# Performance work log

Hardware: AMD Instinct MI355X
Metric: run time of the kernel (lower is better)

Reference implementation:

```python
import jax, jax.numpy as jnp
from jax import lax
import numpy as np

HID = 64      # hidden_size
IND = 25      # input_dim = 10 static + 15 dynamic features
HW = 25       # spatial size fixed by fc1 = Linear(12*12*hidden, ...)


def setup_inputs() -> dict:
    key = jax.random.key(0)
    ks = jax.random.split(key, 8)
    def rn(k, shape, s=0.05):
        return jax.random.normal(k, shape, dtype=jnp.float32) * s
    B, T = 64, 24
    return {
        "x": jax.random.normal(ks[0], (B, T, IND, HW, HW), dtype=jnp.float32),
        "ln_g": jnp.ones((IND,), jnp.float32),
        "ln_b": jnp.zeros((IND,), jnp.float32),
        "w_lstm1": rn(ks[1], (4 * HID, IND + HID, 3, 3)),
        "b_lstm1": jnp.zeros((4 * HID,), jnp.float32),
        "w_lstm2": rn(ks[2], (4 * HID, IND + HID, 3, 3)),
        "b_lstm2": jnp.zeros((4 * HID,), jnp.float32),
        "w_conv": rn(ks[3], (HID, 2 * HID, 3, 3)),
        "b_conv": jnp.zeros((HID,), jnp.float32),
        "w_fc1": rn(ks[4], (HID, 12 * 12 * HID)),
        "b_fc1": jnp.zeros((HID,), jnp.float32),
        "w_fc2": rn(ks[5], (HID // 2, HID)),
        "b_fc2": jnp.zeros((HID // 2,), jnp.float32),
        "w_fc3": rn(ks[6], (2, HID // 2)),
        "b_fc3": jnp.zeros((2,), jnp.float32),
    }


def _convlstm(x, w, b, dil):
    # x: (B, T, C, H, W); one ConvLSTM layer, zero-initialized states.
    # Gate order i, f, o, g (standard ndrplz ConvLSTM); same-padding 3x3 conv
    # with rhs dilation `dil` (padding = dil keeps HxW).
    B, _, _, H, W = x.shape
    h0 = jnp.zeros((B, HID, H, W), x.dtype)

    def step(carry, xt):
        h, c = carry
        z = lax.conv_general_dilated(
            jnp.concatenate([xt, h], axis=1), w, (1, 1),
            [(dil, dil), (dil, dil)], rhs_dilation=(dil, dil))
        z = z + b[None, :, None, None]
        i, f, o, g = jnp.split(z, 4, axis=1)
        c = jax.nn.sigmoid(f) * c + jax.nn.sigmoid(i) * jnp.tanh(g)
        h = jax.nn.sigmoid(o) * jnp.tanh(c)
        return (h, c), None

    (h, _), _ = lax.scan(step, (h0, h0), jnp.moveaxis(x, 1, 0))
    return h  # final hidden state (B, HID, H, W)


def reference(x, ln_g, ln_b, w_lstm1, b_lstm1, w_lstm2, b_lstm2,
              w_conv, b_conv, w_fc1, b_fc1, w_fc2, b_fc2, w_fc3, b_fc3):
    # LayerNorm over the channel dim (torch permutes C to last, LN, permutes back)
    mu = jnp.mean(x, axis=2, keepdims=True)
    var = jnp.var(x, axis=2, keepdims=True)
    xn = (x - mu) * lax.rsqrt(var + 1e-5)
    xn = xn * ln_g[None, None, :, None, None] + ln_b[None, None, :, None, None]

    h1 = _convlstm(xn, w_lstm1, b_lstm1, 1)   # dilation 1 branch
    h2 = _convlstm(xn, w_lstm2, b_lstm2, 2)   # dilation 2 branch
    h = jnp.concatenate([h1, h2], axis=1)     # (B, 2*HID, 25, 25)

    h = lax.conv_general_dilated(h, w_conv, (1, 1), [(1, 1), (1, 1)])
    h = jax.nn.relu(h + b_conv[None, :, None, None])
    # max_pool2d(2): floor(25/2)=12 -> VALID window 2 stride 2
    h = lax.reduce_window(h, -jnp.inf, lax.max, (1, 1, 2, 2), (1, 1, 2, 2), 'VALID')
    h = h.reshape(h.shape[0], -1)             # (B, 12*12*HID), channel-major like torch
    h = jax.nn.relu(h @ w_fc1.T + b_fc1)      # dropout is identity at inference
    h = jax.nn.relu(h @ w_fc2.T + b_fc2)
    h = h @ w_fc3.T + b_fc3
    return jax.nn.log_softmax(h, axis=1)
```

## Files before the change

### kernel.cpp

```cpp
#include <hip/hip_runtime.h>
#include <hip/hip_bf16.h>
#include <math.h>

#define B_    64
#define T_    24
#define IND_  25
#define HID_  64
#define NPIX  625

#define WP0   27
#define WP1   29
#define XSTR  32
#define HSTR  72
#define XROWS0 744
#define XROWS1 856
#define HROWS0 744
#define HROWS1 856
#define XB0   (XROWS0*XSTR)
#define XB1   (XROWS1*XSTR)
#define HB0   (HROWS0*HSTR)
#define HB1   (HROWS1*HSTR)
#define XB0T  (B_*XB0)
#define XB1T  (B_*XB1)
#define HB0T  (B_*HB0)
#define HB1T  (B_*HB1)
#define UEND  (XB0T+XB1T+2*(HB0T+HB1T))

#define RST0  200
#define RST1  272
#define CH0   (RST0*9)
#define CH1   (RST1*9)

#define HCROWS 832
#define HCB    (HCROWS*128)
#define HCTOT  (B_*HCB)

#define WFRAG_PER_BR (9*3*4*4*512)
#define WFRAG_TOT    (2*WFRAG_PER_BR)

typedef __bf16 bf16x8 __attribute__((ext_vector_type(8)));
typedef float  f32x4  __attribute__((ext_vector_type(4)));
typedef unsigned short ushort_t;
typedef unsigned int   uint_t;

typedef const __attribute__((address_space(1))) void as1_cvoid;
typedef __attribute__((address_space(3))) void as3_void;

__device__ __forceinline__ float sigmoidf_(float x) { return 1.f / (1.f + __expf(-x)); }
__device__ __forceinline__ float tanh_fast(float x) { return 2.f / (1.f + __expf(-2.f * x)) - 1.f; }
__device__ __forceinline__ ushort_t f2bf(float f) {
    unsigned int u = __float_as_uint(f);
    u += 0x7FFFu + ((u >> 16) & 1u);
    return (ushort_t)(u >> 16);
}
__device__ __forceinline__ float bf2f(ushort_t h) {
    return __uint_as_float(((unsigned int)h) << 16);
}

__global__ __launch_bounds__(256) void fill_zero_kernel(uint_t* __restrict__ p, int n) {
    int i = blockIdx.x * 256 + threadIdx.x;
    if (i < n) p[i] = 0u;
}

__global__ __launch_bounds__(256) void repack_w_kernel(
    const float* __restrict__ w1, const float* __restrict__ w2, ushort_t* __restrict__ Wfrag)
{
    int id = blockIdx.x * 256 + threadIdx.x;
    if (id >= WFRAG_TOT) return;
    int e    = id & 7;
    int lane = (id >> 3) & 63;
    int mf   = (id >> 9) & 3;
    int wm   = (id >> 11) & 3;
    int rest = id >> 13;
    int kk   = rest % 3;
    int tap  = (rest / 3) % 9;
    int br   = rest / 27;
    int l16 = lane & 15, kh = lane >> 4;
    int gate = mf;
    int oc   = wm * 16 + l16;
    int k    = kh * 8 + e;
    int c;
    if (kk == 0)      c = (k < IND_) ? k : -1;
    else if (kk == 1) c = IND_ + k;
    else              c = IND_ + 32 + k;
    const float* w = br ? w2 : w1;
    float v = (c >= 0) ? w[((size_t)(gate * 64 + oc) * 89 + c) * 9 + tap] : 0.f;
    Wfrag[id] = f2bf(v);
}

__global__ __launch_bounds__(256) void repack_wc_kernel(
    const float* __restrict__ wc, ushort_t* __restrict__ Wc)
{
    int id = blockIdx.x * 256 + threadIdx.x;
    if (id >= 9 * 64 * 128) return;
    int k   = id % 128;
    int oc  = (id / 128) % 64;
    int tap = id / (128 * 64);
    Wc[id] = f2bf(wc[((size_t)(oc * 128) + k) * 9 + tap]);
}

__global__ __launch_bounds__(256) void ln_t_kernel(
    const float* __restrict__ x, const float* __restrict__ gamma, const float* __restrict__ beta,
    ushort_t* __restrict__ xb0, ushort_t* __restrict__ xb1, int t)
{
    int p = blockIdx.x * 256 + threadIdx.x;
    if (p >= B_ * NPIX) return;
    int b = p / NPIX, hw = p % NPIX;
    int y = hw / 25, xx = hw % 25;
    const float* xp = x + ((size_t)(b * T_ + t) * IND_) * NPIX + hw;
    float v[IND_];
    float s = 0.f;
#pragma unroll
    for (int c = 0; c < IND_; ++c) { v[c] = xp[c * NPIX]; s += v[c]; }
    float mu = s * (1.f / IND_);
    float ss = 0.f;
#pragma unroll
    for (int c = 0; c < IND_; ++c) { float d = v[c] - mu; ss += d * d; }
    float rstd = rsqrtf(ss * (1.f / IND_) + 1e-5f);
    ushort_t* o0 = xb0 + (size_t)b * XB0 + (size_t)((y + 1) * WP0 + (xx + 1)) * XSTR;
    ushort_t* o1 = xb1 + (size_t)b * XB1 + (size_t)((y + 2) * WP1 + (xx + 2)) * XSTR;
#pragma unroll
    for (int c = 0; c < IND_; ++c) {
        ushort_t hv = f2bf((v[c] - mu) * rstd * gamma[c] + beta[c]);
        o0[c] = hv;
        o1[c] = hv;
    }
}

__global__ __launch_bounds__(512) void convlstm_mfma_kernel(
    const ushort_t* __restrict__ xb0g, const ushort_t* __restrict__ xb1g,
    const ushort_t* __restrict__ h0c, const ushort_t* __restrict__ h1c,
    ushort_t* __restrict__ h0n, ushort_t* __restrict__ h1n,
    const ushort_t* __restrict__ Wfrag,
    const float* __restrict__ bias1, const float* __restrict__ bias2,
    float* __restrict__ cst, int t)
{
    const int rg = blockIdx.x;
    const int b  = blockIdx.y;
    const int br = blockIdx.z;
    const int d  = 1 + br;
    const int Wp = br ? WP1 : WP0;
    const ushort_t* __restrict__ xb = (br ? xb1g + (size_t)b * XB1 : xb0g + (size_t)b * XB0);
    const ushort_t* __restrict__ hc = (br ? h1c + (size_t)b * HB1 : h0c + (size_t)b * HB0);
    ushort_t* __restrict__ hn       = (br ? h1n + (size_t)b * HB1 : h0n + (size_t)b * HB0);
    const float* __restrict__ bias = br ? bias2 : bias1;
    const ushort_t* __restrict__ WFb = Wfrag + (size_t)br * WFRAG_PER_BR;

    __shared__ ushort_t tile[RST1 * HSTR];

    const int tid = threadIdx.x;
    const int u0  = rg * 5 * Wp;
    const int CH  = br ? CH1 : CH0;

    {
        const char* gsrc = (const char*)(hc + (size_t)u0 * HSTR);
        const int wave_u = tid & 448;
#pragma unroll
        for (int j = 0; j < 5; ++j) {
            const int i = j * 512 + tid;
            if (i < CH) {
                __builtin_amdgcn_global_load_lds(
                    (as1_cvoid*)(gsrc + (size_t)i * 16),
                    (as3_void*)((char*)tile + (size_t)(j * 512 + wave_u) * 16),
                    16, 0, 0);
            }
        }
    }
    __syncthreads();

    const int w    = tid >> 6, lane = tid & 63;
    const int wm   = w & 3, wn = w >> 2;
    const int l16  = lane & 15, kh = lane >> 4;
    const int koff = kh * 8;

    f32x4 acc[4][5];
#pragma unroll
    for (int i = 0; i < 4; ++i)
#pragma unroll
        for (int j = 0; j < 5; ++j) acc[i][j] = (f32x4){0.f, 0.f, 0.f, 0.f};

    int baserel[5];
#pragma unroll
    for (int nf = 0; nf < 5; ++nf) {
        int n = wn * 80 + nf * 16 + l16;
        baserel[nf] = (n >> 5) * Wp + (n & 31);
    }

    for (int tap = 0; tap < 9; ++tap) {
        const int ky = tap / 3, kx = tap - 3 * ky;
        const int toff = (ky * Wp + kx) * d;
        const ushort_t* __restrict__ WT = WFb + (size_t)(tap * 3) * 8192 + wm * 2048 + lane * 8;

        {
            bf16x8 af[4], bfr[5];
#pragma unroll
            for (int mf = 0; mf < 4; ++mf)
                af[mf] = *(const bf16x8*)(WT + mf * 512);
#pragma unroll
            for (int nf = 0; nf < 5; ++nf)
                bfr[nf] = *(const bf16x8*)(xb + (size_t)(u0 + baserel[nf] + toff) * XSTR + koff);
#pragma unroll
            for (int mf = 0; mf < 4; ++mf)
#pragma unroll
                for (int nf = 0; nf < 5; ++nf)
                    acc[mf][nf] = __builtin_amdgcn_mfma_f32_16x16x32_bf16(
                        af[mf], bfr[nf], acc[mf][nf], 0, 0, 0);
        }
#pragma unroll
        for (int kkh = 0; kkh < 2; ++kkh) {
            bf16x8 af[4], bfr[5];
#pragma unroll
            for (int mf = 0; mf < 4; ++mf)
                af[mf] = *(const bf16x8*)(WT + (size_t)(kkh + 1) * 8192 + mf * 512);
#pragma unroll
            for (int nf = 0; nf < 5; ++nf)
                bfr[nf] = *(const bf16x8*)(tile + (baserel[nf] + toff) * HSTR + kkh * 32 + koff);
#pragma unroll
            for (int mf = 0; mf < 4; ++mf)
#pragma unroll
                for (int nf = 0; nf < 5; ++nf)
                    acc[mf][nf] = __builtin_amdgcn_mfma_f32_16x16x32_bf16(
                        af[mf], bfr[nf], acc[mf][nf], 0, 0, 0);
        }
    }

    const int oc0 = wm * 16 + kh * 4;
    float bi4[4], bf4[4], bo4[4], bg4[4];
#pragma unroll
    for (int r = 0; r < 4; ++r) {
        bi4[r] = bias[oc0 + r];
        bf4[r] = bias[64 + oc0 + r];
        bo4[r] = bias[128 + oc0 + r];
        bg4[r] = bias[192 + oc0 + r];
    }
#pragma unroll
    for (int nf = 0; nf < 5; ++nf) {
        const int n = wn * 80 + nf * 16 + l16;
        const int xx = n & 31;
        if (xx >= 25) continue;
        const int y = rg * 5 + (n >> 5);
        const int pix = y * 25 + xx;
        const size_t cbase = ((size_t)((br * B_ + b) * HID_) + oc0) * NPIX + pix;
        ushort_t hs[4];
#pragma unroll
        for (int r = 0; r < 4; ++r) {
            const float zi = acc[0][nf][r] + bi4[r];
            const float zf = acc[1][nf][r] + bf4[r];
            const float zo = acc[2][nf][r] + bo4[r];
            const float zg = acc[3][nf][r] + bg4[r];
            float co = 0.f;
            if (t != 0) co = cst[cbase + (size_t)r * NPIX];
            const float cn = sigmoidf_(zf) * co + sigmoidf_(zi) * tanh_fast(zg);
            cst[cbase + (size_t)r * NPIX] = cn;
            hs[r] = f2bf(sigmoidf_(zo) * tanh_fast(cn));
        }
        uint2 hv;
        hv.x = (uint_t)hs[0] | ((uint_t)hs[1] << 16);
        hv.y = (uint_t)hs[2] | ((uint_t)hs[3] << 16);
        *(uint2*)(hn + (size_t)((y + d) * Wp + (xx + d)) * HSTR + oc0) = hv;
    }
}

__global__ __launch_bounds__(256) void combine_h_kernel(
    const ushort_t* __restrict__ h0, const ushort_t* __restrict__ h1, ushort_t* __restrict__ Hc)
{
    int id = blockIdx.x * 256 + threadIdx.x;
    if (id >= B_ * NPIX * 128) return;
    int k   = id % 128;
    int pix = (id / 128) % NPIX;
    int b   = id / (128 * NPIX);
    int y = pix / 25, xx = pix % 25;
    ushort_t v;
    if (k < 64) v = h0[(size_t)b * HB0 + (size_t)((y + 1) * WP0 + (xx + 1)) * HSTR + k];
    else        v = h1[(size_t)b * HB1 + (size_t)((y + 2) * WP1 + (xx + 2)) * HSTR + (k - 64)];
    Hc[(size_t)b * HCB + (size_t)((y + 1) * 27 + (xx + 1)) * 128 + k] = v;
}

__global__ __launch_bounds__(512) void conv_mfma_kernel(
    const ushort_t* __restrict__ Hc, const ushort_t* __restrict__ Wc,
    const float* __restrict__ bc, float* __restrict__ conv_out)
{
    const int rg = blockIdx.x;
    const int b  = blockIdx.y;
    const ushort_t* __restrict__ Hb = Hc + (size_t)b * HCB;

    const int tid  = threadIdx.x;
    const int w    = tid >> 6, lane = tid & 63;
    const int wm   = w & 1, wn = w >> 1;
    const int l16  = lane & 15, kh = lane >> 4;
    const int koff = kh * 8;

    f32x4 acc[2][2];
#pragma unroll
    for (int i = 0; i < 2; ++i)
#pragma unroll
        for (int j = 0; j < 2; ++j) acc[i][j] = (f32x4){0.f, 0.f, 0.f, 0.f};

    int baserow[2];
#pragma unroll
    for (int nf = 0; nf < 2; ++nf) {
        int n = wn * 32 + nf * 16 + l16;
        baserow[nf] = (rg * 4 + (n >> 5)) * 27 + (n & 31);
    }
    const ushort_t* __restrict__ Wm = Wc + (size_t)(wm * 32 + l16) * 128 + koff;

    for (int tap = 0; tap < 9; ++tap) {
        const int ky = tap / 3, kx = tap - 3 * ky;
        const int toff = ky * 27 + kx;
        const ushort_t* __restrict__ Wt = Wm + (size_t)tap * (64 * 128);
        const ushort_t* Urow[2];
#pragma unroll
        for (int nf = 0; nf < 2; ++nf)
            Urow[nf] = Hb + (size_t)(baserow[nf] + toff) * 128 + koff;
#pragma unroll
        for (int kk = 0; kk < 4; ++kk) {
            bf16x8 af[2], bfr[2];
#pragma unroll
            for (int mf = 0; mf < 2; ++mf)
                af[mf] = *(const bf16x8*)(Wt + mf * 16 * 128 + kk * 32);
#pragma unroll
            for (int nf = 0; nf < 2; ++nf)
                bfr[nf] = *(const bf16x8*)(Urow[nf] + kk * 32);
#pragma unroll
            for (int mf = 0; mf < 2; ++mf)
#pragma unroll
                for (int nf = 0; nf < 2; ++nf)
                    acc[mf][nf] = __builtin_amdgcn_mfma_f32_16x16x32_bf16(
                        af[mf], bfr[nf], acc[mf][nf], 0, 0, 0);
        }
    }

#pragma unroll
    for (int mf = 0; mf < 2; ++mf) {
#pragma unroll
        for (int nf = 0; nf < 2; ++nf) {
            const int n = wn * 32 + nf * 16 + l16;
            const int xx = n & 31;
            if (xx >= 25) continue;
            const int y = rg * 4 + wn;
            if (y >= 25) continue;
#pragma unroll
            for (int r = 0; r < 4; ++r) {
                const int oc = wm * 32 + mf * 16 + kh * 4 + r;
                const float v = fmaxf(acc[mf][nf][r] + bc[oc], 0.f);
                conv_out[((size_t)(b * 64 + oc)) * NPIX + y * 25 + xx] = v;
            }
        }
    }
}

__global__ __launch_bounds__(256) void pool_kernel(
    const float* __restrict__ conv_out, float* __restrict__ pool)
{
    int id = blockIdx.x * 256 + threadIdx.x;
    if (id >= B_ * 64 * 144) return;
    int px = id % 12;
    int py = (id / 12) % 12;
    int oc = (id / 144) % 64;
    int b  = id / (144 * 64);
    const float* p = conv_out + ((size_t)(b * 64 + oc)) * NPIX;
    const int cy = 2 * py, cx = 2 * px;
    float mx = fmaxf(fmaxf(p[cy * 25 + cx], p[cy * 25 + cx + 1]),
                     fmaxf(p[(cy + 1) * 25 + cx], p[(cy + 1) * 25 + cx + 1]));
    pool[(size_t)b * 9216 + oc * 144 + py * 12 + px] = mx;
}

__global__ __launch_bounds__(256) void fc1_kernel(
    const float* __restrict__ pool, const float* __restrict__ w1, const float* __restrict__ b1,
    float* __restrict__ f1)
{
    const int task = blockIdx.x * 4 + (threadIdx.x >> 6);
    const int lane = threadIdx.x & 63;
    const int b = task >> 6, oc = task & 63;
    const float* pr = pool + (size_t)b * 9216;
    const float* wr = w1 + (size_t)oc * 9216;
    float acc = 0.f;
#pragma unroll 4
    for (int it = 0; it < 36; ++it) {
        const int k = it * 256 + lane * 4;
        const float4 p = *(const float4*)(pr + k);
        const float4 ww = *(const float4*)(wr + k);
        acc += p.x * ww.x + p.y * ww.y + p.z * ww.z + p.w * ww.w;
    }
#pragma unroll
    for (int off = 32; off > 0; off >>= 1) acc += __shfl_down(acc, off);
    if (lane == 0) f1[b * 64 + oc] = fmaxf(acc + b1[oc], 0.f);
}

__global__ __launch_bounds__(64) void head2_kernel(
    const float* __restrict__ f1,
    const float* __restrict__ w2, const float* __restrict__ b2,
    const float* __restrict__ w3, const float* __restrict__ b3,
    float* __restrict__ out)
{
    const int b = blockIdx.x;
    __shared__ float f1l[64];
    __shared__ float f2[32];
    const int tid = threadIdx.x;
    f1l[tid] = f1[b * 64 + tid];
    __syncthreads();
    if (tid < 32) {
        float acc = b2[tid];
        const float* wr = w2 + (size_t)tid * 64;
#pragma unroll
        for (int k = 0; k < 64; ++k) acc += f1l[k] * wr[k];
        f2[tid] = fmaxf(acc, 0.f);
    }
    __syncthreads();
    if (tid == 0) {
        float y0 = b3[0], y1 = b3[1];
#pragma unroll
        for (int k = 0; k < 32; ++k) { y0 += f2[k] * w3[k]; y1 += f2[k] * w3[32 + k]; }
        const float m = fmaxf(y0, y1);
        const float lse = m + logf(expf(y0 - m) + expf(y1 - m));
        out[b * 2 + 0] = y0 - lse;
        out[b * 2 + 1] = y1 - lse;
    }
}

extern "C" void kernel_launch(void* const* d_in, const int* in_sizes, int n_in,
                              void* d_out, int out_size, void* d_ws, size_t ws_size,
                              hipStream_t stream) {
    const float* x    = (const float*)d_in[0];
    const float* ln_g = (const float*)d_in[1];
    const float* ln_b = (const float*)d_in[2];
    const float* w_l1 = (const float*)d_in[3];
    const float* b_l1 = (const float*)d_in[4];
    const float* w_l2 = (const float*)d_in[5];
    const float* b_l2 = (const float*)d_in[6];
    const float* w_c  = (const float*)d_in[7];
    const float* b_c  = (const float*)d_in[8];
    const float* w_f1 = (const float*)d_in[9];
    const float* b_f1 = (const float*)d_in[10];
    const float* w_f2 = (const float*)d_in[11];
    const float* b_f2 = (const float*)d_in[12];
    const float* w_f3 = (const float*)d_in[13];
    const float* b_f3 = (const float*)d_in[14];

    ushort_t* wsu = (ushort_t*)d_ws;
    uint_t*   wsi = (uint_t*)d_ws;

    ushort_t* xb0 = wsu;
    ushort_t* xb1 = xb0 + XB0T;
    ushort_t* h0A = xb1 + XB1T;
    ushort_t* h1A = h0A + HB0T;
    ushort_t* h0B = h1A + HB1T;
    ushort_t* h1B = h0B + HB0T;
    float*    cst = (float*)(wsu + UEND);
    float*    conv_out = cst;
    float*    pool = cst + 2560000;
    ushort_t* Wfrag = wsu + UEND + 10240000;
    ushort_t* Wc    = Wfrag + WFRAG_TOT;
    float*    f1    = (float*)(Wc + 73728);
    ushort_t* Hc    = h0B;

    fill_zero_kernel<<<(UEND / 2 + 255) / 256, 256, 0, stream>>>(wsi, UEND / 2);
    repack_w_kernel<<<(WFRAG_TOT + 255) / 256, 256, 0, stream>>>(w_l1, w_l2, Wfrag);
    repack_wc_kernel<<<(9 * 64 * 128 + 255) / 256, 256, 0, stream>>>(w_c, Wc);

    ushort_t* H0[2] = {h0A, h0B};
    ushort_t* H1[2] = {h1A, h1B};
    for (int t = 0; t < T_; ++t) {
        const int cur = t & 1, nxt = cur ^ 1;
        ln_t_kernel<<<(B_ * NPIX + 255) / 256, 256, 0, stream>>>(x, ln_g, ln_b, xb0, xb1, t);
        convlstm_mfma_kernel<<<dim3(5, B_, 2), 512, 0, stream>>>(
            xb0, xb1, H0[cur], H1[cur], H0[nxt], H1[nxt], Wfrag, b_l1, b_l2, cst, t);
    }
    fill_zero_kernel<<<(HCTOT / 2 + 255) / 256, 256, 0, stream>>>((uint_t*)Hc, HCTOT / 2);
    combine_h_kernel<<<(B_ * NPIX * 128 + 255) / 256, 256, 0, stream>>>(h0A, h1A, Hc);
    conv_mfma_kernel<<<dim3(7, B_), 512, 0, stream>>>(Hc, Wc, b_c, conv_out);
    pool_kernel<<<(B_ * 64 * 144 + 255) / 256, 256, 0, stream>>>(conv_out, pool);
    fc1_kernel<<<1024, 256, 0, stream>>>(pool, w_f1, b_f1, f1);
    head2_kernel<<<B_, 64, 0, stream>>>(f1, w_f2, b_f2, w_f3, b_f3, (float*)d_out);
}
```

Measured before the change: 2.266 ms.

## Fuse ConvLSTM timesteps into persistent cooperative kernel with register-resident cell state

Replaces the 48 per-timestep launches (layer norm plus ConvLSTM) with one cooperative persistent kernel of 256 blocks. Each block processes 2-3 tiles per step, uses grid.sync between steps, and keeps the cell state in registers instead of global memory. It also overlaps the next step's layer norm and the next tile's LDS staging with the current MFMA work, double-buffering both the x buffers and the LDS tile. The aims are to remove launch overhead and cell-state memory traffic. The costs are grid-wide barriers, higher register pressure, and an occupancy requirement of 2 blocks per CU.

```diff
diff --git a/kernel.cpp b/kernel.cpp
--- a/kernel.cpp
+++ b/kernel.cpp
@@ -1,6 +1,9 @@
 #include <hip/hip_runtime.h>
 #include <hip/hip_bf16.h>
+#include <hip/hip_cooperative_groups.h>
 #include <math.h>
+
+namespace cg = cooperative_groups;
 
 #define B_    64
 #define T_    24
@@ -24,7 +27,7 @@
 #define XB1T  (B_*XB1)
 #define HB0T  (B_*HB0)
 #define HB1T  (B_*HB1)
-#define UEND  (XB0T+XB1T+2*(HB0T+HB1T))
+#define HPART (HB0T+HB1T)
 
 #define RST0  200
 #define RST1  272
@@ -99,79 +102,89 @@
     Wc[id] = f2bf(wc[((size_t)(oc * 128) + k) * 9 + tap]);
 }
 
-__global__ __launch_bounds__(256) void ln_t_kernel(
+
+__device__ __forceinline__ void ln_phase(
     const float* __restrict__ x, const float* __restrict__ gamma, const float* __restrict__ beta,
-    ushort_t* __restrict__ xb0, ushort_t* __restrict__ xb1, int t)
-{
-    int p = blockIdx.x * 256 + threadIdx.x;
+    ushort_t* __restrict__ xb, int tt, int bid, int tid)
+{
+    if (tid >= 157) return;
+    const int p = bid * 157 + tid;
     if (p >= B_ * NPIX) return;
-    int b = p / NPIX, hw = p % NPIX;
-    int y = hw / 25, xx = hw % 25;
-    const float* xp = x + ((size_t)(b * T_ + t) * IND_) * NPIX + hw;
+    const int b = p / NPIX, hw = p - b * NPIX;
+    const int y = hw / 25, xx = hw - y * 25;
+    const float* xp = x + ((size_t)(b * T_ + tt) * IND_) * NPIX + hw;
     float v[IND_];
     float s = 0.f;
 #pragma unroll
     for (int c = 0; c < IND_; ++c) { v[c] = xp[c * NPIX]; s += v[c]; }
-    float mu = s * (1.f / IND_);
+    const float mu = s * (1.f / IND_);
     float ss = 0.f;
 #pragma unroll
-    for (int c = 0; c < IND_; ++c) { float d = v[c] - mu; ss += d * d; }
-    float rstd = rsqrtf(ss * (1.f / IND_) + 1e-5f);
-    ushort_t* o0 = xb0 + (size_t)b * XB0 + (size_t)((y + 1) * WP0 + (xx + 1)) * XSTR;
-    ushort_t* o1 = xb1 + (size_t)b * XB1 + (size_t)((y + 2) * WP1 + (xx + 2)) * XSTR;
-#pragma unroll
-    for (int c = 0; c < IND_; ++c) {
-        ushort_t hv = f2bf((v[c] - mu) * rstd * gamma[c] + beta[c]);
-        o0[c] = hv;
-        o1[c] = hv;
-    }
-}
-
-__global__ __launch_bounds__(512) void convlstm_mfma_kernel(
-    const ushort_t* __restrict__ xb0g, const ushort_t* __restrict__ xb1g,
-    const ushort_t* __restrict__ h0c, const ushort_t* __restrict__ h1c,
-    ushort_t* __restrict__ h0n, ushort_t* __restrict__ h1n,
+    for (int c = 0; c < IND_; ++c) { float dd = v[c] - mu; ss += dd * dd; }
+    const float rstd = rsqrtf(ss * (1.f / IND_) + 1e-5f);
+    ushort_t us[IND_];
+#pragma unroll
+    for (int c = 0; c < IND_; ++c) us[c] = f2bf((v[c] - mu) * rstd * gamma[c] + beta[c]);
+    uint4 q0, q1, q2;
+    q0.x = us[0] | ((uint_t)us[1] << 16);  q0.y = us[2] | ((uint_t)us[3] << 16);
+    q0.z = us[4] | ((uint_t)us[5] << 16);  q0.w = us[6] | ((uint_t)us[7] << 16);
+    q1.x = us[8] | ((uint_t)us[9] << 16);  q1.y = us[10] | ((uint_t)us[11] << 16);
+    q1.z = us[12] | ((uint_t)us[13] << 16); q1.w = us[14] | ((uint_t)us[15] << 16);
+    q2.x = us[16] | ((uint_t)us[17] << 16); q2.y = us[18] | ((uint_t)us[19] << 16);
+    q2.z = us[20] | ((uint_t)us[21] << 16); q2.w = us[22] | ((uint_t)us[23] << 16);
+    const int par = tt & 1;
+    ushort_t* o0 = xb + (size_t)par * XB0T + (size_t)b * XB0 + (size_t)((y + 1) * WP0 + (xx + 1)) * XSTR;
+    ushort_t* o1 = xb + 2 * (size_t)XB0T + (size_t)par * XB1T + (size_t)b * XB1 + (size_t)((y + 2) * WP1 + (xx + 2)) * XSTR;
+    *(uint4*)o0 = q0; *(uint4*)(o0 + 8) = q1; *(uint4*)(o0 + 16) = q2; o0[24] = us[24];
+    *(uint4*)o1 = q0; *(uint4*)(o1 + 8) = q1; *(uint4*)(o1 + 16) = q2; o1[24] = us[24];
+}
+
+__device__ __forceinline__ void stage_tile(
+    int tile, int cur, int tid, const ushort_t* __restrict__ hb, ushort_t* ldsbuf)
+{
+    const int rg = tile % 5, b = (tile / 5) & 63, br = tile / 320;
+    const int Wp = 25 + 2 * (1 + br);
+    const ushort_t* hc = hb + (size_t)cur * HPART +
+                         (br ? (size_t)HB0T + (size_t)b * HB1 : (size_t)b * HB0);
+    const int u0 = rg * 5 * Wp;
+    const int CH = br ? CH1 : CH0;
+    const char* gsrc = (const char*)(hc + (size_t)u0 * HSTR);
+    const int wave_u = tid & 448;
+#pragma unroll
+    for (int j = 0; j < 5; ++j) {
+        const int i = j * 512 + tid;
+        if (i < CH) {
+            __builtin_amdgcn_global_load_lds(
+                (as1_cvoid*)(gsrc + (size_t)i * 16),
+                (as3_void*)((char*)ldsbuf + (size_t)(j * 512 + wave_u) * 16),
+                16, 0, 0);
+        }
+    }
+}
+
+__device__ __forceinline__ void conv_tile(
+    int tile, int cur, int nxt, int tid,
+    const ushort_t* __restrict__ xb, ushort_t* __restrict__ hb,
     const ushort_t* __restrict__ Wfrag,
     const float* __restrict__ bias1, const float* __restrict__ bias2,
-    float* __restrict__ cst, int t)
-{
-    const int rg = blockIdx.x;
-    const int b  = blockIdx.y;
-    const int br = blockIdx.z;
-    const int d  = 1 + br;
-    const int Wp = br ? WP1 : WP0;
-    const ushort_t* __restrict__ xb = (br ? xb1g + (size_t)b * XB1 : xb0g + (size_t)b * XB0);
-    const ushort_t* __restrict__ hc = (br ? h1c + (size_t)b * HB1 : h0c + (size_t)b * HB0);
-    ushort_t* __restrict__ hn       = (br ? h1n + (size_t)b * HB1 : h0n + (size_t)b * HB0);
+    const ushort_t* __restrict__ lds, f32x4 (&cacc)[5])
+{
+    const int rg = tile % 5, b = (tile / 5) & 63, br = tile / 320;
+    const int d = 1 + br;
+    const int Wp = 25 + 2 * d;
+    const ushort_t* __restrict__ xbuf =
+        xb + (br ? 2 * (size_t)XB0T + (size_t)cur * XB1T + (size_t)b * XB1
+                 : (size_t)cur * XB0T + (size_t)b * XB0);
+    ushort_t* __restrict__ hnx =
+        hb + (size_t)nxt * HPART + (br ? (size_t)HB0T + (size_t)b * HB1 : (size_t)b * HB0);
     const float* __restrict__ bias = br ? bias2 : bias1;
     const ushort_t* __restrict__ WFb = Wfrag + (size_t)br * WFRAG_PER_BR;
-
-    __shared__ ushort_t tile[RST1 * HSTR];
-
-    const int tid = threadIdx.x;
-    const int u0  = rg * 5 * Wp;
-    const int CH  = br ? CH1 : CH0;
-
-    {
-        const char* gsrc = (const char*)(hc + (size_t)u0 * HSTR);
-        const int wave_u = tid & 448;
-#pragma unroll
-        for (int j = 0; j < 5; ++j) {
-            const int i = j * 512 + tid;
-            if (i < CH) {
-                __builtin_amdgcn_global_load_lds(
-                    (as1_cvoid*)(gsrc + (size_t)i * 16),
-                    (as3_void*)((char*)tile + (size_t)(j * 512 + wave_u) * 16),
-                    16, 0, 0);
-            }
-        }
-    }
-    __syncthreads();
 
     const int w    = tid >> 6, lane = tid & 63;
     const int wm   = w & 3, wn = w >> 2;
     const int l16  = lane & 15, kh = lane >> 4;
     const int koff = kh * 8;
+    const int u0   = rg * 5 * Wp;
 
     f32x4 acc[4][5];
 #pragma unroll
@@ -190,7 +203,6 @@
         const int ky = tap / 3, kx = tap - 3 * ky;
         const int toff = (ky * Wp + kx) * d;
         const ushort_t* __restrict__ WT = WFb + (size_t)(tap * 3) * 8192 + wm * 2048 + lane * 8;
-
         {
             bf16x8 af[4], bfr[5];
 #pragma unroll
@@ -198,7 +210,7 @@
                 af[mf] = *(const bf16x8*)(WT + mf * 512);
 #pragma unroll
             for (int nf = 0; nf < 5; ++nf)
-                bfr[nf] = *(const bf16x8*)(xb + (size_t)(u0 + baserel[nf] + toff) * XSTR + koff);
+                bfr[nf] = *(const bf16x8*)(xbuf + (size_t)(u0 + baserel[nf] + toff) * XSTR + koff);
 #pragma unroll
             for (int mf = 0; mf < 4; ++mf)
 #pragma unroll
@@ -214,7 +226,7 @@
                 af[mf] = *(const bf16x8*)(WT + (size_t)(kkh + 1) * 8192 + mf * 512);
 #pragma unroll
             for (int nf = 0; nf < 5; ++nf)
-                bfr[nf] = *(const bf16x8*)(tile + (baserel[nf] + toff) * HSTR + kkh * 32 + koff);
+                bfr[nf] = *(const bf16x8*)(lds + (baserel[nf] + toff) * HSTR + kkh * 32 + koff);
 #pragma unroll
             for (int mf = 0; mf < 4; ++mf)
 #pragma unroll
@@ -239,8 +251,6 @@
         const int xx = n & 31;
         if (xx >= 25) continue;
         const int y = rg * 5 + (n >> 5);
-        const int pix = y * 25 + xx;
-        const size_t cbase = ((size_t)((br * B_ + b) * HID_) + oc0) * NPIX + pix;
         ushort_t hs[4];
 #pragma unroll
         for (int r = 0; r < 4; ++r) {
@@ -248,18 +258,57 @@
             const float zf = acc[1][nf][r] + bf4[r];
             const float zo = acc[2][nf][r] + bo4[r];
             const float zg = acc[3][nf][r] + bg4[r];
-            float co = 0.f;
-            if (t != 0) co = cst[cbase + (size_t)r * NPIX];
-            const float cn = sigmoidf_(zf) * co + sigmoidf_(zi) * tanh_fast(zg);
-            cst[cbase + (size_t)r * NPIX] = cn;
+            const float cn = sigmoidf_(zf) * cacc[nf][r] + sigmoidf_(zi) * tanh_fast(zg);
+            cacc[nf][r] = cn;
             hs[r] = f2bf(sigmoidf_(zo) * tanh_fast(cn));
         }
         uint2 hv;
         hv.x = (uint_t)hs[0] | ((uint_t)hs[1] << 16);
         hv.y = (uint_t)hs[2] | ((uint_t)hs[3] << 16);
-        *(uint2*)(hn + (size_t)((y + d) * Wp + (xx + d)) * HSTR + oc0) = hv;
-    }
-}
+        *(uint2*)(hnx + (size_t)((y + d) * Wp + (xx + d)) * HSTR + oc0) = hv;
+    }
+}
+
+__global__ __launch_bounds__(512, 2) void persist_kernel(
+    const float* __restrict__ x, const float* __restrict__ ln_g, const float* __restrict__ ln_b,
+    ushort_t* __restrict__ xb, ushort_t* __restrict__ hb, const ushort_t* __restrict__ Wfrag,
+    const float* __restrict__ b_l1, const float* __restrict__ b_l2)
+{
+    cg::grid_group grid = cg::this_grid();
+    const int bid = blockIdx.x, tid = threadIdx.x;
+    const bool has2 = (bid < 128);
+
+    __shared__ ushort_t lds[2][RST1 * HSTR];
+
+    f32x4 c0[5], c1[5], c2[5];
+#pragma unroll
+    for (int j = 0; j < 5; ++j) {
+        c0[j] = (f32x4){0.f, 0.f, 0.f, 0.f};
+        c1[j] = (f32x4){0.f, 0.f, 0.f, 0.f};
+        c2[j] = (f32x4){0.f, 0.f, 0.f, 0.f};
+    }
+
+    ln_phase(x, ln_g, ln_b, xb, 0, bid, tid);
+    grid.sync();
+
+    for (int t = 0; t < T_; ++t) {
+        const int cur = t & 1, nxt = cur ^ 1;
+        stage_tile(bid, cur, tid, hb, lds[0]);
+        if (t + 1 < T_) ln_phase(x, ln_g, ln_b, xb, t + 1, bid, tid);
+        __syncthreads();
+        stage_tile(bid + 256, cur, tid, hb, lds[1]);
+        conv_tile(bid, cur, nxt, tid, xb, hb, Wfrag, b_l1, b_l2, lds[0], c0);
+        __syncthreads();
+        if (has2) stage_tile(bid + 512, cur, tid, hb, lds[0]);
+        conv_tile(bid + 256, cur, nxt, tid, xb, hb, Wfrag, b_l1, b_l2, lds[1], c1);
+        if (has2) {
+            __syncthreads();
+            conv_tile(bid + 512, cur, nxt, tid, xb, hb, Wfrag, b_l1, b_l2, lds[0], c2);
+        }
+        grid.sync();
+    }
+}
+
 
 __global__ __launch_bounds__(256) void combine_h_kernel(
     const ushort_t* __restrict__ h0, const ushort_t* __restrict__ h1, ushort_t* __restrict__ Hc)
@@ -440,34 +489,28 @@
     ushort_t* wsu = (ushort_t*)d_ws;
     uint_t*   wsi = (uint_t*)d_ws;
 
-    ushort_t* xb0 = wsu;
-    ushort_t* xb1 = xb0 + XB0T;
-    ushort_t* h0A = xb1 + XB1T;
-    ushort_t* h1A = h0A + HB0T;
-    ushort_t* h0B = h1A + HB1T;
-    ushort_t* h1B = h0B + HB0T;
-    float*    cst = (float*)(wsu + UEND);
-    float*    conv_out = cst;
-    float*    pool = cst + 2560000;
-    ushort_t* Wfrag = wsu + UEND + 10240000;
+    ushort_t* xb    = wsu;
+    ushort_t* hb    = wsu + 2 * (size_t)XB0T + 2 * (size_t)XB1T;
+    ushort_t* Wfrag = hb + 2 * (size_t)HPART;
     ushort_t* Wc    = Wfrag + WFRAG_TOT;
     float*    f1    = (float*)(Wc + 73728);
-    ushort_t* Hc    = h0B;
-
-    fill_zero_kernel<<<(UEND / 2 + 255) / 256, 256, 0, stream>>>(wsi, UEND / 2);
+    ushort_t* Hc    = hb + HPART;
+    float*    conv_out = (float*)wsu;
+    float*    pool  = (float*)wsu + 2560000;
+
+    const int n_fill = (int)((2 * (size_t)XB0T + 2 * (size_t)XB1T + 2 * (size_t)HPART) / 2);
+    fill_zero_kernel<<<(n_fill + 255) / 256, 256, 0, stream>>>(wsi, n_fill);
     repack_w_kernel<<<(WFRAG_TOT + 255) / 256, 256, 0, stream>>>(w_l1, w_l2, Wfrag);
     repack_wc_kernel<<<(9 * 64 * 128 + 255) / 256, 256, 0, stream>>>(w_c, Wc);
 
-    ushort_t* H0[2] = {h0A, h0B};
-    ushort_t* H1[2] = {h1A, h1B};
-    for (int t = 0; t < T_; ++t) {
-        const int cur = t & 1, nxt = cur ^ 1;
-        ln_t_kernel<<<(B_ * NPIX + 255) / 256, 256, 0, stream>>>(x, ln_g, ln_b, xb0, xb1, t);
-        convlstm_mfma_kernel<<<dim3(5, B_, 2), 512, 0, stream>>>(
-            xb0, xb1, H0[cur], H1[cur], H0[nxt], H1[nxt], Wfrag, b_l1, b_l2, cst, t);
-    }
+    void* kargs[8];
+    kargs[0] = (void*)&x;    kargs[1] = (void*)&ln_g; kargs[2] = (void*)&ln_b;
+    kargs[3] = (void*)&xb;   kargs[4] = (void*)&hb;   kargs[5] = (void*)&Wfrag;
+    kargs[6] = (void*)&b_l1; kargs[7] = (void*)&b_l2;
+    hipLaunchCooperativeKernel((void*)persist_kernel, dim3(256), dim3(512), kargs, 0, stream);
+
     fill_zero_kernel<<<(HCTOT / 2 + 255) / 256, 256, 0, stream>>>((uint_t*)Hc, HCTOT / 2);
-    combine_h_kernel<<<(B_ * NPIX * 128 + 255) / 256, 256, 0, stream>>>(h0A, h1A, Hc);
+    combine_h_kernel<<<(B_ * NPIX * 128 + 255) / 256, 256, 0, stream>>>(hb, hb + HB0T, Hc);
     conv_mfma_kernel<<<dim3(7, B_), 512, 0, stream>>>(Hc, Wc, b_c, conv_out);
     pool_kernel<<<(B_ * 64 * 144 + 255) / 256, 256, 0, stream>>>(conv_out, pool);
     fc1_kernel<<<1024, 256, 0, stream>>>(pool, w_f1, b_f1, f1);
```

Measured after the change: 3.591 ms. +58.4%, slower.
